# Kernel tuning notes

Hardware: AMD Instinct MI355X
Metric: run time of the kernel (lower is better)

## Reference

```python
import jax, jax.numpy as jnp
import numpy as np

N_NODES = 64
N_EDGES = N_NODES * (N_NODES - 1)  # 4032 (fully connected, no self-loops)
BATCH = 64
N_IN = 64
N_HID = 128
N_OUT = 16


def _linear_params(key, fan_in, fan_out):
    # mimic torch nn.Linear default init: U(-1/sqrt(fan_in), 1/sqrt(fan_in))
    kw, kb = jax.random.split(key)
    s = 1.0 / np.sqrt(fan_in)
    W = jax.random.uniform(kw, (fan_in, fan_out), minval=-s, maxval=s, dtype=jnp.float32)
    b = jax.random.uniform(kb, (fan_out,), minval=-s, maxval=s, dtype=jnp.float32)
    return W, b


def setup_inputs() -> dict:
    key = jax.random.key(0)
    ks = jax.random.split(key, 10)
    # one-hot relation matrices for fully-connected graph without self loops
    pairs = np.array([(i, j) for i in range(N_NODES) for j in range(N_NODES) if i != j])
    eye = np.eye(N_NODES, dtype=np.float32)
    rel_send = jnp.asarray(eye[pairs[:, 0]])  # [E, N]
    rel_rec = jnp.asarray(eye[pairs[:, 1]])   # [E, N]

    x = jax.random.normal(ks[0], (BATCH, N_NODES, N_IN), dtype=jnp.float32)

    w1a, b1a = _linear_params(ks[1], N_IN, N_HID)
    w1b, b1b = _linear_params(ks[2], N_HID, N_HID)
    w2a, b2a = _linear_params(ks[3], 2 * N_HID, N_HID)
    w2b, b2b = _linear_params(ks[4], N_HID, N_HID)
    w3a, b3a = _linear_params(ks[5], N_HID, N_HID)
    w3b, b3b = _linear_params(ks[6], N_HID, N_HID)
    w4a, b4a = _linear_params(ks[7], 3 * N_HID, N_HID)  # factor=True
    w4b, b4b = _linear_params(ks[8], N_HID, N_HID)
    wout, bout = _linear_params(ks[9], N_HID, N_OUT)

    return dict(x=x, rel_rec=rel_rec, rel_send=rel_send,
                w1a=w1a, b1a=b1a, w1b=w1b, b1b=b1b,
                w2a=w2a, b2a=b2a, w2b=w2b, b2b=b2b,
                w3a=w3a, b3a=b3a, w3b=w3b, b3b=b3b,
                w4a=w4a, b4a=b4a, w4b=w4b, b4b=b4b,
                wout=wout, bout=bout)


def _mlp(x, wa, ba, wb, bb):
    # Linear -> ReLU -> Linear
    return jax.nn.relu(x @ wa + ba) @ wb + bb


def reference(x, rel_rec, rel_send,
              w1a, b1a, w1b, b1b,
              w2a, b2a, w2b, b2b,
              w3a, b3a, w3b, b3b,
              w4a, b4a, w4b, b4b,
              wout, bout):
    def node2edge(h):
        receivers = jnp.einsum('en,bnh->beh', rel_rec, h)
        senders = jnp.einsum('en,bnh->beh', rel_send, h)
        return jnp.concatenate([senders, receivers], axis=-1)  # [B,E,2H]

    def edge2node(e):
        agg = jnp.einsum('en,beh->bnh', rel_rec, e)
        norm = rel_rec.sum(0)[None, :, None]  # [1,N,1]
        return agg / (norm + 1e-6)

    h = _mlp(x, w1a, b1a, w1b, b1b)            # [B,N,H]
    e = _mlp(node2edge(h), w2a, b2a, w2b, b2b)  # [B,E,H]
    x_skip = e
    # factor=True branch
    n = _mlp(edge2node(e), w3a, b3a, w3b, b3b)  # [B,N,H]
    e2 = node2edge(n)                           # [B,E,2H]
    e2 = jnp.concatenate([e2, x_skip], axis=2)  # [B,E,3H]
    e2 = _mlp(e2, w4a, b4a, w4b, b4b)           # [B,E,H]
    return e2 @ wout + bout                     # [B,E,n_out]
```

## Files before the change

### kernel.cpp

```cpp
#include <hip/hip_runtime.h>
#include <hip/hip_bf16.h>


#define DI __device__ __forceinline__

typedef short bf16x8 __attribute__((ext_vector_type(8)));
typedef float f32x4 __attribute__((ext_vector_type(4)));
typedef unsigned short u16;
typedef unsigned long long u64;

static constexpr int NN = 64, NE = 4032, H = 128;

DI u16 f2bf(float f) {
  union { float f; unsigned u; } v; v.f = f;
  unsigned u = v.u;
  return (u16)((u + 0x7fffu + ((u >> 16) & 1u)) >> 16);
}
DI unsigned pk2(float a, float b) {
  union { __hip_bfloat162 h; unsigned u; } c;
  c.h = __float22bfloat162_rn(float2{a, b});
  return c.u;
}
DI f32x4 mf(bf16x8 a, bf16x8 b, f32x4 c) {
  return __builtin_amdgcn_mfma_f32_16x16x32_bf16(a, b, c, 0, 0, 0);
}
DI bf16x8 ldfrag(const u16* __restrict__ p, int idx, int l) {
  return *reinterpret_cast<const bf16x8*>(p + (idx * 64 + l) * 8);
}

__global__ __launch_bounds__(64) void prepack_kernel(
    const float* __restrict__ w1a, const float* __restrict__ w1b,
    const float* __restrict__ w2a, const float* __restrict__ w2b,
    const float* __restrict__ w3a, const float* __restrict__ w3b,
    const float* __restrict__ w4a, const float* __restrict__ w4b,
    const float* __restrict__ wout,
    const float* __restrict__ b2b, const float* __restrict__ b4b,
    const float* __restrict__ bout,
    u16* __restrict__ pk, float* __restrict__ c2, float* __restrict__ c4) {
  int seg = blockIdx.y, f = blockIdx.x, l = threadIdx.x;
  int h = l >> 4, mm = l & 15;
  if (seg == 10) {
    if (f >= 4) return;
    union { u16 u[8]; uint4 q; } o;
#pragma unroll
    for (int jj = 0; jj < 8; jj++) {
      int row = f * 32 + h * 8 + jj;
      float s0 = 0.f, s1 = 0.f, s2 = 0.f, s3 = 0.f;
      for (int j = 0; j < 128; j += 4) {
        s0 += w4b[row * 128 + j]     * wout[j * 16 + mm];
        s1 += w4b[row * 128 + j + 1] * wout[(j + 1) * 16 + mm];
        s2 += w4b[row * 128 + j + 2] * wout[(j + 2) * 16 + mm];
        s3 += w4b[row * 128 + j + 3] * wout[(j + 3) * 16 + mm];
      }
      o.u[jj] = f2bf((s0 + s1) + (s2 + s3));
    }
    *reinterpret_cast<uint4*>(pk + ((304 + f) * 64 + l) * 8) = o.q;
    return;
  }
  if (seg == 11) {
    if (f < 2) {
      int o = f * 64 + l;
      float s0 = 0.f, s1 = 0.f;
      for (int k = 0; k < 128; k += 2) {
        s0 += b2b[k] * w4a[(256 + k) * 128 + o];
        s1 += b2b[k + 1] * w4a[(256 + k + 1) * 128 + o];
      }
      c2[o] = s0 + s1;
    } else if (f == 2 && l < 16) {
      float s = bout[l];
      for (int k = 0; k < 128; k++) s += b4b[k] * wout[k * 16 + l];
      c4[l] = s;
    }
    return;
  }
  const float* src; int foff, nfrag, roff, pi;
  switch (seg) {
    case 0:  src = w1a; foff = 0;   nfrag = 16; roff = 0;   pi = 0; break;
    case 1:  src = w1b; foff = 16;  nfrag = 32; roff = 0;   pi = 1; break;
    case 2:  src = w2a; foff = 48;  nfrag = 32; roff = 0;   pi = 1; break;
    case 3:  src = w2a; foff = 80;  nfrag = 32; roff = 128; pi = 1; break;
    case 4:  src = w2b; foff = 112; nfrag = 32; roff = 0;   pi = 0; break;
    case 5:  src = w3a; foff = 144; nfrag = 32; roff = 0;   pi = 1; break;
    case 6:  src = w3b; foff = 176; nfrag = 32; roff = 0;   pi = 1; break;
    case 7:  src = w4a; foff = 208; nfrag = 32; roff = 0;   pi = 1; break;
    case 8:  src = w4a; foff = 240; nfrag = 32; roff = 128; pi = 1; break;
    default: src = w4a; foff = 272; nfrag = 32; roff = 256; pi = 0; break;
  }
  if (f >= nfrag) return;
  int kt = f >> 3, ct = f & 7;
  union { u16 u[8]; uint4 q; } o;
#pragma unroll
  for (int jj = 0; jj < 8; jj++) {
    int row = pi ? (kt * 32 + (jj >> 2) * 16 + h * 4 + (jj & 3))
                 : (kt * 32 + h * 8 + jj);
    o.u[jj] = f2bf(src[(roff + row) * 128 + ct * 16 + mm]);
  }
  *reinterpret_cast<uint4*>(pk + ((foff + f) * 64 + l) * 8) = o.q;
}

__global__ __launch_bounds__(512, 2) void node_kernel(
    const float* __restrict__ x, const u16* __restrict__ pk,
    const float* __restrict__ b1a, const float* __restrict__ b1b,
    const float* __restrict__ b2a,
    float* __restrict__ sproj, float* __restrict__ rproj) {
  __shared__ bf16x8 act[2][4][64];
  int blk = blockIdx.x, b = blk >> 2, nq = blk & 3;
  int tid = threadIdx.x, l = tid & 63, w = tid >> 6;
  int m = l & 15, h = l >> 4;
  int node = nq * 16 + m;
  const f32x4 Z = {0.f, 0.f, 0.f, 0.f};
  bf16x8 wpre[14];
  wpre[0] = ldfrag(pk, w, l);
  wpre[1] = ldfrag(pk, 8 + w, l);
#pragma unroll
  for (int kt = 0; kt < 4; kt++) {
    wpre[2 + kt]  = ldfrag(pk + 16 * 512, kt * 8 + w, l);
    wpre[6 + kt]  = ldfrag(pk + 48 * 512, kt * 8 + w, l);
    wpre[10 + kt] = ldfrag(pk + 80 * 512, kt * 8 + w, l);
  }
  f32x4 acc;
  {
    const float* xb = x + (b * NN + node) * 64;
    bf16x8 xin[2];
#pragma unroll
    for (int kt = 0; kt < 2; kt++) {
      f32x4 a0 = *(const f32x4*)(xb + kt * 32 + h * 8);
      f32x4 a1 = *(const f32x4*)(xb + kt * 32 + h * 8 + 4);
      union { unsigned u[4]; bf16x8 v; } t;
      t.u[0] = pk2(a0[0], a0[1]); t.u[1] = pk2(a0[2], a0[3]);
      t.u[2] = pk2(a1[0], a1[1]); t.u[3] = pk2(a1[2], a1[3]);
      xin[kt] = t.v;
    }
    acc = mf(wpre[0], xin[0], Z);
    acc = mf(wpre[1], xin[1], acc);
    f32x4 bb = *(const f32x4*)(b1a + w * 16 + h * 4);
    union { unsigned u[2]; u64 d; } p;
    p.u[0] = pk2(fmaxf(acc[0] + bb[0], 0.f), fmaxf(acc[1] + bb[1], 0.f));
    p.u[1] = pk2(fmaxf(acc[2] + bb[2], 0.f), fmaxf(acc[3] + bb[3], 0.f));
    reinterpret_cast<u64*>(&act[0][w >> 1][l])[w & 1] = p.d;
  }
  __syncthreads();
  bf16x8 ef[4];
#pragma unroll
  for (int kt = 0; kt < 4; kt++) ef[kt] = act[0][kt][l];
#pragma unroll
  for (int kt = 0; kt < 4; kt++)
    acc = mf(wpre[2 + kt], ef[kt], kt == 0 ? Z : acc);
  {
    f32x4 bb = *(const f32x4*)(b1b + w * 16 + h * 4);
    union { unsigned u[2]; u64 d; } p;
    p.u[0] = pk2(acc[0] + bb[0], acc[1] + bb[1]);
    p.u[1] = pk2(acc[2] + bb[2], acc[3] + bb[3]);
    reinterpret_cast<u64*>(&act[1][w >> 1][l])[w & 1] = p.d;
  }
  __syncthreads();
#pragma unroll
  for (int kt = 0; kt < 4; kt++) ef[kt] = act[1][kt][l];
#pragma unroll
  for (int kt = 0; kt < 4; kt++)
    acc = mf(wpre[6 + kt], ef[kt], kt == 0 ? Z : acc);
  *reinterpret_cast<f32x4*>(sproj + (b * NN + node) * H + w * 16 + h * 4) = acc;
#pragma unroll
  for (int kt = 0; kt < 4; kt++)
    acc = mf(wpre[10 + kt], ef[kt], kt == 0 ? Z : acc);
  {
    f32x4 bb = *(const f32x4*)(b2a + w * 16 + h * 4);
    f32x4 o = acc;
    o[0] += bb[0]; o[1] += bb[1]; o[2] += bb[2]; o[3] += bb[3];
    *reinterpret_cast<f32x4*>(rproj + (b * NN + node) * H + w * 16 + h * 4) = o;
  }
}

__global__ __launch_bounds__(512, 2) void agg_kernel(
    const float* __restrict__ sproj, const float* __restrict__ rproj,
    const u16* __restrict__ pk,
    const float* __restrict__ b2b, const float* __restrict__ b3a,
    const float* __restrict__ b3b, const float* __restrict__ b4a,
    const float* __restrict__ c2,
    float* __restrict__ s4, float* __restrict__ r4) {
  __shared__ f32x4 lred[8][8][64];
  __shared__ bf16x8 act[2][4][64];
  int blk = blockIdx.x, b = blk >> 2, jq = blk & 3;
  int tid = threadIdx.x, l = tid & 63, w = tid >> 6, m = l & 15, h = l >> 4;
  int j = jq * 16 + m;
  const float* rpb = rproj + (b * NN + j) * H;
  f32x4 rpv[8], accS[8];
#pragma unroll
  for (int k = 0; k < 8; k++) {
    rpv[k] = *(const f32x4*)(rpb + (k >> 1) * 32 + h * 8 + (k & 1) * 4);
    accS[k] = f32x4{0.f, 0.f, 0.f, 0.f};
  }
  const float* spb = sproj + b * NN * H;
  for (int i = w * 8; i < w * 8 + 8; i++) {
    const float* sp = spb + i * H;
#pragma unroll
    for (int k = 0; k < 8; k++) {
      f32x4 s = *(const f32x4*)(sp + (k >> 1) * 32 + h * 8 + (k & 1) * 4);
      f32x4 t = s + rpv[k];
      t[0] = fmaxf(t[0], 0.f); t[1] = fmaxf(t[1], 0.f);
      t[2] = fmaxf(t[2], 0.f); t[3] = fmaxf(t[3], 0.f);
      accS[k] += t;
    }
  }
  if ((j >> 3) == w) {
    const float* sp = spb + j * H;
#pragma unroll
    for (int k = 0; k < 8; k++) {
      f32x4 s = *(const f32x4*)(sp + (k >> 1) * 32 + h * 8 + (k & 1) * 4);
      f32x4 t = s + rpv[k];
      accS[k][0] -= fmaxf(t[0], 0.f); accS[k][1] -= fmaxf(t[1], 0.f);
      accS[k][2] -= fmaxf(t[2], 0.f); accS[k][3] -= fmaxf(t[3], 0.f);
    }
  }
#pragma unroll
  for (int k = 0; k < 8; k++) lred[w][k][l] = accS[k];
  bf16x8 wpre[20];
#pragma unroll
  for (int kt = 0; kt < 4; kt++) {
    wpre[kt]      = ldfrag(pk + 112 * 512, kt * 8 + w, l);
    wpre[4 + kt]  = ldfrag(pk + 144 * 512, kt * 8 + w, l);
    wpre[8 + kt]  = ldfrag(pk + 176 * 512, kt * 8 + w, l);
    wpre[12 + kt] = ldfrag(pk + 208 * 512, kt * 8 + w, l);
    wpre[16 + kt] = ldfrag(pk + 240 * 512, kt * 8 + w, l);
  }
  __syncthreads();
  if (w < 4) {
    f32x4 s0 = f32x4{0.f, 0.f, 0.f, 0.f}, s1 = s0;
#pragma unroll
    for (int ww = 0; ww < 8; ww++) {
      s0 += lred[ww][2 * w][l];
      s1 += lred[ww][2 * w + 1][l];
    }
    union { unsigned u[4]; bf16x8 v; } t;
    t.u[0] = pk2(s0[0], s0[1]); t.u[1] = pk2(s0[2], s0[3]);
    t.u[2] = pk2(s1[0], s1[1]); t.u[3] = pk2(s1[2], s1[3]);
    act[0][w][l] = t.v;
  }
  __syncthreads();
  const f32x4 Z = {0.f, 0.f, 0.f, 0.f};
  f32x4 acc;
  bf16x8 ef[4];
#pragma unroll
  for (int kt = 0; kt < 4; kt++) ef[kt] = act[0][kt][l];
#pragma unroll
  for (int kt = 0; kt < 4; kt++)
    acc = mf(wpre[kt], ef[kt], kt == 0 ? Z : acc);
  {
    const float inv = 1.0f / (63.0f + 1e-6f);
    const float binv = 63.0f * inv;
    f32x4 bb = *(const f32x4*)(b2b + w * 16 + h * 4);
    union { unsigned u[2]; u64 d; } p;
    p.u[0] = pk2(acc[0] * inv + bb[0] * binv, acc[1] * inv + bb[1] * binv);
    p.u[1] = pk2(acc[2] * inv + bb[2] * binv, acc[3] * inv + bb[3] * binv);
    reinterpret_cast<u64*>(&act[1][w >> 1][l])[w & 1] = p.d;
  }
  __syncthreads();
#pragma unroll
  for (int kt = 0; kt < 4; kt++) ef[kt] = act[1][kt][l];
#pragma unroll
  for (int kt = 0; kt < 4; kt++)
    acc = mf(wpre[4 + kt], ef[kt], kt == 0 ? Z : acc);
  {
    f32x4 bb = *(const f32x4*)(b3a + w * 16 + h * 4);
    union { unsigned u[2]; u64 d; } p;
    p.u[0] = pk2(fmaxf(acc[0] + bb[0], 0.f), fmaxf(acc[1] + bb[1], 0.f));
    p.u[1] = pk2(fmaxf(acc[2] + bb[2], 0.f), fmaxf(acc[3] + bb[3], 0.f));
    reinterpret_cast<u64*>(&act[0][w >> 1][l])[w & 1] = p.d;
  }
  __syncthreads();
#pragma unroll
  for (int kt = 0; kt < 4; kt++) ef[kt] = act[0][kt][l];
#pragma unroll
  for (int kt = 0; kt < 4; kt++)
    acc = mf(wpre[8 + kt], ef[kt], kt == 0 ? Z : acc);
  {
    f32x4 bb = *(const f32x4*)(b3b + w * 16 + h * 4);
    union { unsigned u[2]; u64 d; } p;
    p.u[0] = pk2(acc[0] + bb[0], acc[1] + bb[1]);
    p.u[1] = pk2(acc[2] + bb[2], acc[3] + bb[3]);
    reinterpret_cast<u64*>(&act[1][w >> 1][l])[w & 1] = p.d;
  }
  __syncthreads();
#pragma unroll
  for (int kt = 0; kt < 4; kt++) ef[kt] = act[1][kt][l];
#pragma unroll
  for (int kt = 0; kt < 4; kt++)
    acc = mf(wpre[12 + kt], ef[kt], kt == 0 ? Z : acc);
  {
    f32x4 cc = *(const f32x4*)(c2 + w * 16 + h * 4);
    f32x4 o = acc;
    o[0] += cc[0]; o[1] += cc[1]; o[2] += cc[2]; o[3] += cc[3];
    *reinterpret_cast<f32x4*>(s4 + (b * NN + j) * H + w * 16 + h * 4) = o;
  }
#pragma unroll
  for (int kt = 0; kt < 4; kt++)
    acc = mf(wpre[16 + kt], ef[kt], kt == 0 ? Z : acc);
  {
    f32x4 bb = *(const f32x4*)(b4a + w * 16 + h * 4);
    f32x4 o = acc;
    o[0] += bb[0]; o[1] += bb[1]; o[2] += bb[2]; o[3] += bb[3];
    *reinterpret_cast<f32x4*>(r4 + (b * NN + j) * H + w * 16 + h * 4) = o;
  }
}

__global__ __launch_bounds__(256, 4) void edge_kernel(
    const float* __restrict__ sproj, const float* __restrict__ rproj,
    const float* __restrict__ s4, const float* __restrict__ r4,
    const u16* __restrict__ pk, const float* __restrict__ c4,
    float* __restrict__ out) {
  __shared__ alignas(16) u16 bufA[8192];
  __shared__ alignas(16) u16 bufB[8192];
  int blk = blockIdx.x;
  int wg = (blk & 7) * 512 + (blk >> 3);
  int b = wg >> 6, i = wg & 63;
  int tid = threadIdx.x, l = tid & 63, w = tid >> 6;
  int m16 = l & 15, h = l >> 4;
  const f32x4 Z = {0.f, 0.f, 0.f, 0.f};
  int jnv[4];
#pragma unroll
  for (int n = 0; n < 4; n++) {
    int e = n * 16 + m16;
    int v = e + (e >= i ? 1 : 0); jnv[n] = v > 63 ? 63 : v;
  }
  {
    const float* spp = sproj + (b * NN + i) * H + w * 32 + h * 8;
    f32x4 s0 = *(const f32x4*)spp, s1 = *(const f32x4*)(spp + 4);
#pragma unroll
    for (int n = 0; n < 4; n++) {
      const float* rpp = rproj + (b * NN + jnv[n]) * H + w * 32 + h * 8;
      f32x4 r0 = *(const f32x4*)rpp, r1 = *(const f32x4*)(rpp + 4);
      union { unsigned u[4]; uint4 q; } t;
      t.u[0] = pk2(fmaxf(s0[0] + r0[0], 0.f), fmaxf(s0[1] + r0[1], 0.f));
      t.u[1] = pk2(fmaxf(s0[2] + r0[2], 0.f), fmaxf(s0[3] + r0[3], 0.f));
      t.u[2] = pk2(fmaxf(s1[0] + r1[0], 0.f), fmaxf(s1[1] + r1[1], 0.f));
      t.u[3] = pk2(fmaxf(s1[2] + r1[2], 0.f), fmaxf(s1[3] + r1[3], 0.f));
      *reinterpret_cast<uint4*>(&bufA[((w * 4 + n) * 64 + l) * 8]) = t.q;
    }
  }
  bf16x8 wv[8];
#pragma unroll
  for (int idx = 0; idx < 8; idx++)
    wv[idx] = ldfrag(pk + 112 * 512, (idx >> 1) * 8 + 2 * w + (idx & 1), l);
  __syncthreads();
  f32x4 acc[2][4];
  __builtin_amdgcn_s_setprio(1);
#pragma unroll
  for (int n = 0; n < 4; n++) {
    bf16x8 bf[4];
#pragma unroll
    for (int kt = 0; kt < 4; kt++)
      bf[kt] = *reinterpret_cast<const bf16x8*>(&bufA[((kt * 4 + n) * 64 + l) * 8]);
#pragma unroll
    for (int kt = 0; kt < 4; kt++)
#pragma unroll
      for (int m = 0; m < 2; m++)
        acc[m][n] = mf(wv[kt * 2 + m], bf[kt], kt == 0 ? Z : acc[m][n]);
  }
  __builtin_amdgcn_s_setprio(0);
#pragma unroll
  for (int idx = 0; idx < 8; idx++)
    wv[idx] = ldfrag(pk + 272 * 512, (idx >> 1) * 8 + 2 * w + (idx & 1), l);
  {
    int lane2b = (h >> 1) * 16 + m16;
    int jb = (h & 1) * 4;
#pragma unroll
    for (int m = 0; m < 2; m++)
#pragma unroll
      for (int n = 0; n < 4; n++) {
        union { unsigned u[2]; u64 d; } p;
        p.u[0] = pk2(acc[m][n][0], acc[m][n][1]);
        p.u[1] = pk2(acc[m][n][2], acc[m][n][3]);
        *reinterpret_cast<u64*>(
            &bufB[((w * 4 + n) * 64 + lane2b + m * 32) * 8 + jb]) = p.d;
      }
  }
  f32x4 s4v[2], rv[4][2];
#pragma unroll
  for (int m = 0; m < 2; m++)
    s4v[m] = *(const f32x4*)(s4 + (b * NN + i) * H + w * 32 + m * 16 + h * 4);
#pragma unroll
  for (int n = 0; n < 4; n++) {
    const float* r4p = r4 + (b * NN + jnv[n]) * H + w * 32 + h * 4;
#pragma unroll
    for (int m = 0; m < 2; m++) rv[n][m] = *(const f32x4*)(r4p + m * 16);
  }
  __syncthreads();
  __builtin_amdgcn_s_setprio(1);
#pragma unroll
  for (int n = 0; n < 4; n++) {
    bf16x8 bf[4];
#pragma unroll
    for (int kt = 0; kt < 4; kt++)
      bf[kt] = *reinterpret_cast<const bf16x8*>(&bufB[((kt * 4 + n) * 64 + l) * 8]);
#pragma unroll
    for (int kt = 0; kt < 4; kt++)
#pragma unroll
      for (int m = 0; m < 2; m++)
        acc[m][n] = mf(wv[kt * 2 + m], bf[kt], kt == 0 ? Z : acc[m][n]);
  }
  __builtin_amdgcn_s_setprio(0);
  {
    int lane2b = (h >> 1) * 16 + m16;
    int jb = (h & 1) * 4;
#pragma unroll
    for (int n = 0; n < 4; n++)
#pragma unroll
      for (int m = 0; m < 2; m++) {
        f32x4 r = rv[n][m];
        union { unsigned u[2]; u64 d; } p;
        p.u[0] = pk2(fmaxf(acc[m][n][0] + s4v[m][0] + r[0], 0.f),
                     fmaxf(acc[m][n][1] + s4v[m][1] + r[1], 0.f));
        p.u[1] = pk2(fmaxf(acc[m][n][2] + s4v[m][2] + r[2], 0.f),
                     fmaxf(acc[m][n][3] + s4v[m][3] + r[3], 0.f));
        *reinterpret_cast<u64*>(
            &bufA[((w * 4 + n) * 64 + lane2b + m * 32) * 8 + jb]) = p.d;
      }
  }
  __syncthreads();
  {
    bf16x8 wfv[4], bf[4];
#pragma unroll
    for (int kt = 0; kt < 4; kt++) {
      wfv[kt] = ldfrag(pk + 304 * 512, kt, l);
      bf[kt] = *reinterpret_cast<const bf16x8*>(&bufA[((kt * 4 + w) * 64 + l) * 8]);
    }
    f32x4 a4 = Z;
#pragma unroll
    for (int kt = 0; kt < 4; kt++) a4 = mf(wfv[kt], bf[kt], a4);
    int jj = w * 16 + m16;
    if (jj < 63) {
      f32x4 c4v = *(const f32x4*)(c4 + h * 4);
      f32x4 o;
      o[0] = a4[0] + c4v[0]; o[1] = a4[1] + c4v[1];
      o[2] = a4[2] + c4v[2]; o[3] = a4[3] + c4v[3];
      *reinterpret_cast<f32x4*>(out + (b * NE + i * 63 + jj) * 16 + h * 4) = o;
    }
  }
}

extern "C" void kernel_launch(void* const* d_in, const int* in_sizes, int n_in,
                              void* d_out, int out_size, void* d_ws, size_t ws_size,
                              hipStream_t stream) {
  const float* x    = (const float*)d_in[0];
  const float* w1a  = (const float*)d_in[3];
  const float* b1a  = (const float*)d_in[4];
  const float* w1b  = (const float*)d_in[5];
  const float* b1b  = (const float*)d_in[6];
  const float* w2a  = (const float*)d_in[7];
  const float* b2a  = (const float*)d_in[8];
  const float* w2b  = (const float*)d_in[9];
  const float* b2b  = (const float*)d_in[10];
  const float* w3a  = (const float*)d_in[11];
  const float* b3a  = (const float*)d_in[12];
  const float* w3b  = (const float*)d_in[13];
  const float* b3b  = (const float*)d_in[14];
  const float* w4a  = (const float*)d_in[15];
  const float* b4a  = (const float*)d_in[16];
  const float* w4b  = (const float*)d_in[17];
  const float* b4b  = (const float*)d_in[18];
  const float* wout = (const float*)d_in[19];
  const float* bout = (const float*)d_in[20];
  float* out = (float*)d_out;

  float* sproj = (float*)d_ws;
  float* rproj = sproj + 524288;
  float* s4    = rproj + 524288;
  float* r4    = s4 + 524288;
  u16* pkw     = (u16*)(r4 + 524288);
  float* c2    = (float*)(pkw + 174080);
  float* c4    = c2 + 128;

  prepack_kernel<<<dim3(32, 12), 64, 0, stream>>>(
      w1a, w1b, w2a, w2b, w3a, w3b, w4a, w4b, wout, b2b, b4b, bout, pkw, c2, c4);
  node_kernel<<<256, 512, 0, stream>>>(x, pkw, b1a, b1b, b2a, sproj, rproj);
  agg_kernel<<<256, 512, 0, stream>>>(sproj, rproj, pkw, b2b, b3a, b3b, b4a, c2, s4, r4);
  edge_kernel<<<4096, 256, 0, stream>>>(sproj, rproj, s4, r4, pkw, c4, out);
}
```

Before: 83.31 us.

## Process four sender nodes per edge block with software-pipelined staging

Each edge_kernel block now handles four consecutive sender nodes in a loop instead of one, cutting the grid from 4096 to 1024 blocks. The next sender's first-layer input is loaded from global memory and written to a third LDS buffer while the current sender's second and third GEMMs run. The aim is to amortize block launch and weight-fragment setup and to hide global load latency. In exchange, LDS use rises to 48KB per block, which may lower occupancy, and there are fewer blocks to spread across CUs.

```diff
diff --git a/kernel.cpp b/kernel.cpp
--- a/kernel.cpp
+++ b/kernel.cpp
@@ -308,132 +308,164 @@
     const float* __restrict__ s4, const float* __restrict__ r4,
     const u16* __restrict__ pk, const float* __restrict__ c4,
     float* __restrict__ out) {
-  __shared__ alignas(16) u16 bufA[8192];
-  __shared__ alignas(16) u16 bufB[8192];
+  __shared__ alignas(16) u16 bufT[8192];
+  __shared__ alignas(16) u16 bufE[8192];
+  __shared__ alignas(16) u16 bufU[8192];
   int blk = blockIdx.x;
-  int wg = (blk & 7) * 512 + (blk >> 3);
-  int b = wg >> 6, i = wg & 63;
+  int wg = (blk & 7) * 128 + (blk >> 3);
+  int b = wg >> 4, sg = wg & 15;
   int tid = threadIdx.x, l = tid & 63, w = tid >> 6;
   int m16 = l & 15, h = l >> 4;
   const f32x4 Z = {0.f, 0.f, 0.f, 0.f};
-  int jnv[4];
-#pragma unroll
-  for (int n = 0; n < 4; n++) {
-    int e = n * 16 + m16;
-    int v = e + (e >= i ? 1 : 0); jnv[n] = v > 63 ? 63 : v;
-  }
-  {
-    const float* spp = sproj + (b * NN + i) * H + w * 32 + h * 8;
+  int i0 = sg * 4;
+  {
+    const float* spp = sproj + (b * NN + i0) * H + w * 32 + h * 8;
     f32x4 s0 = *(const f32x4*)spp, s1 = *(const f32x4*)(spp + 4);
 #pragma unroll
     for (int n = 0; n < 4; n++) {
-      const float* rpp = rproj + (b * NN + jnv[n]) * H + w * 32 + h * 8;
+      int e = n * 16 + m16;
+      int v = e + (e >= i0 ? 1 : 0); v = v > 63 ? 63 : v;
+      const float* rpp = rproj + (b * NN + v) * H + w * 32 + h * 8;
       f32x4 r0 = *(const f32x4*)rpp, r1 = *(const f32x4*)(rpp + 4);
       union { unsigned u[4]; uint4 q; } t;
       t.u[0] = pk2(fmaxf(s0[0] + r0[0], 0.f), fmaxf(s0[1] + r0[1], 0.f));
       t.u[1] = pk2(fmaxf(s0[2] + r0[2], 0.f), fmaxf(s0[3] + r0[3], 0.f));
       t.u[2] = pk2(fmaxf(s1[0] + r1[0], 0.f), fmaxf(s1[1] + r1[1], 0.f));
       t.u[3] = pk2(fmaxf(s1[2] + r1[2], 0.f), fmaxf(s1[3] + r1[3], 0.f));
-      *reinterpret_cast<uint4*>(&bufA[((w * 4 + n) * 64 + l) * 8]) = t.q;
-    }
-  }
-  bf16x8 wv[8];
-#pragma unroll
-  for (int idx = 0; idx < 8; idx++)
-    wv[idx] = ldfrag(pk + 112 * 512, (idx >> 1) * 8 + 2 * w + (idx & 1), l);
-  __syncthreads();
-  f32x4 acc[2][4];
-  __builtin_amdgcn_s_setprio(1);
-#pragma unroll
-  for (int n = 0; n < 4; n++) {
-    bf16x8 bf[4];
-#pragma unroll
-    for (int kt = 0; kt < 4; kt++)
-      bf[kt] = *reinterpret_cast<const bf16x8*>(&bufA[((kt * 4 + n) * 64 + l) * 8]);
-#pragma unroll
-    for (int kt = 0; kt < 4; kt++)
+      *reinterpret_cast<uint4*>(&bufT[((w * 4 + n) * 64 + l) * 8]) = t.q;
+    }
+  }
+  __syncthreads();
+#pragma unroll 1
+  for (int s = 0; s < 4; s++) {
+    int i = i0 + s;
+    int jnv[4];
+#pragma unroll
+    for (int n = 0; n < 4; n++) {
+      int e = n * 16 + m16;
+      int v = e + (e >= i ? 1 : 0); jnv[n] = v > 63 ? 63 : v;
+    }
+    f32x4 acc[2][4];
+    bf16x8 wv[8];
+#pragma unroll
+    for (int idx = 0; idx < 8; idx++)
+      wv[idx] = ldfrag(pk + 112 * 512, (idx >> 1) * 8 + 2 * w + (idx & 1), l);
+    __builtin_amdgcn_s_setprio(1);
+#pragma unroll
+    for (int n = 0; n < 4; n++) {
+      bf16x8 bf[4];
+#pragma unroll
+      for (int kt = 0; kt < 4; kt++)
+        bf[kt] = *reinterpret_cast<const bf16x8*>(&bufT[((kt * 4 + n) * 64 + l) * 8]);
+#pragma unroll
+      for (int kt = 0; kt < 4; kt++)
+#pragma unroll
+        for (int m = 0; m < 2; m++)
+          acc[m][n] = mf(wv[kt * 2 + m], bf[kt], kt == 0 ? Z : acc[m][n]);
+    }
+    __builtin_amdgcn_s_setprio(0);
+#pragma unroll
+    for (int idx = 0; idx < 8; idx++)
+      wv[idx] = ldfrag(pk + 272 * 512, (idx >> 1) * 8 + 2 * w + (idx & 1), l);
+    {
+      int lane2b = (h >> 1) * 16 + m16;
+      int jb = (h & 1) * 4;
 #pragma unroll
       for (int m = 0; m < 2; m++)
-        acc[m][n] = mf(wv[kt * 2 + m], bf[kt], kt == 0 ? Z : acc[m][n]);
-  }
-  __builtin_amdgcn_s_setprio(0);
-#pragma unroll
-  for (int idx = 0; idx < 8; idx++)
-    wv[idx] = ldfrag(pk + 272 * 512, (idx >> 1) * 8 + 2 * w + (idx & 1), l);
-  {
-    int lane2b = (h >> 1) * 16 + m16;
-    int jb = (h & 1) * 4;
+#pragma unroll
+        for (int n = 0; n < 4; n++) {
+          union { unsigned u[2]; u64 d; } p;
+          p.u[0] = pk2(acc[m][n][0], acc[m][n][1]);
+          p.u[1] = pk2(acc[m][n][2], acc[m][n][3]);
+          *reinterpret_cast<u64*>(
+              &bufE[((w * 4 + n) * 64 + lane2b + m * 32) * 8 + jb]) = p.d;
+        }
+    }
+    f32x4 ts0, ts1, tr[4][2];
+    if (s < 3) {
+      int i2 = i + 1;
+      const float* spp = sproj + (b * NN + i2) * H + w * 32 + h * 8;
+      ts0 = *(const f32x4*)spp; ts1 = *(const f32x4*)(spp + 4);
+#pragma unroll
+      for (int n = 0; n < 4; n++) {
+        int e = n * 16 + m16;
+        int v = e + (e >= i2 ? 1 : 0); v = v > 63 ? 63 : v;
+        const float* rpp = rproj + (b * NN + v) * H + w * 32 + h * 8;
+        tr[n][0] = *(const f32x4*)rpp; tr[n][1] = *(const f32x4*)(rpp + 4);
+      }
+    }
+    __syncthreads();
+    if (s < 3) {
+#pragma unroll
+      for (int n = 0; n < 4; n++) {
+        union { unsigned u[4]; uint4 q; } t;
+        t.u[0] = pk2(fmaxf(ts0[0] + tr[n][0][0], 0.f), fmaxf(ts0[1] + tr[n][0][1], 0.f));
+        t.u[1] = pk2(fmaxf(ts0[2] + tr[n][0][2], 0.f), fmaxf(ts0[3] + tr[n][0][3], 0.f));
+        t.u[2] = pk2(fmaxf(ts1[0] + tr[n][1][0], 0.f), fmaxf(ts1[1] + tr[n][1][1], 0.f));
+        t.u[3] = pk2(fmaxf(ts1[2] + tr[n][1][2], 0.f), fmaxf(ts1[3] + tr[n][1][3], 0.f));
+        *reinterpret_cast<uint4*>(&bufT[((w * 4 + n) * 64 + l) * 8]) = t.q;
+      }
+    }
+    f32x4 s4v[2], rv[4][2];
 #pragma unroll
     for (int m = 0; m < 2; m++)
-#pragma unroll
-      for (int n = 0; n < 4; n++) {
-        union { unsigned u[2]; u64 d; } p;
-        p.u[0] = pk2(acc[m][n][0], acc[m][n][1]);
-        p.u[1] = pk2(acc[m][n][2], acc[m][n][3]);
-        *reinterpret_cast<u64*>(
-            &bufB[((w * 4 + n) * 64 + lane2b + m * 32) * 8 + jb]) = p.d;
+      s4v[m] = *(const f32x4*)(s4 + (b * NN + i) * H + w * 32 + m * 16 + h * 4);
+#pragma unroll
+    for (int n = 0; n < 4; n++) {
+      const float* r4p = r4 + (b * NN + jnv[n]) * H + w * 32 + h * 4;
+#pragma unroll
+      for (int m = 0; m < 2; m++) rv[n][m] = *(const f32x4*)(r4p + m * 16);
+    }
+    __builtin_amdgcn_s_setprio(1);
+#pragma unroll
+    for (int n = 0; n < 4; n++) {
+      bf16x8 bf[4];
+#pragma unroll
+      for (int kt = 0; kt < 4; kt++)
+        bf[kt] = *reinterpret_cast<const bf16x8*>(&bufE[((kt * 4 + n) * 64 + l) * 8]);
+#pragma unroll
+      for (int kt = 0; kt < 4; kt++)
+#pragma unroll
+        for (int m = 0; m < 2; m++)
+          acc[m][n] = mf(wv[kt * 2 + m], bf[kt], kt == 0 ? Z : acc[m][n]);
+    }
+    __builtin_amdgcn_s_setprio(0);
+    {
+      int lane2b = (h >> 1) * 16 + m16;
+      int jb = (h & 1) * 4;
+#pragma unroll
+      for (int n = 0; n < 4; n++)
+#pragma unroll
+        for (int m = 0; m < 2; m++) {
+          f32x4 r = rv[n][m];
+          union { unsigned u[2]; u64 d; } p;
+          p.u[0] = pk2(fmaxf(acc[m][n][0] + s4v[m][0] + r[0], 0.f),
+                       fmaxf(acc[m][n][1] + s4v[m][1] + r[1], 0.f));
+          p.u[1] = pk2(fmaxf(acc[m][n][2] + s4v[m][2] + r[2], 0.f),
+                       fmaxf(acc[m][n][3] + s4v[m][3] + r[3], 0.f));
+          *reinterpret_cast<u64*>(
+              &bufU[((w * 4 + n) * 64 + lane2b + m * 32) * 8 + jb]) = p.d;
+        }
+    }
+    __syncthreads();
+    {
+      bf16x8 wfv[4], bf[4];
+#pragma unroll
+      for (int kt = 0; kt < 4; kt++) {
+        wfv[kt] = ldfrag(pk + 304 * 512, kt, l);
+        bf[kt] = *reinterpret_cast<const bf16x8*>(&bufU[((kt * 4 + w) * 64 + l) * 8]);
       }
-  }
-  f32x4 s4v[2], rv[4][2];
-#pragma unroll
-  for (int m = 0; m < 2; m++)
-    s4v[m] = *(const f32x4*)(s4 + (b * NN + i) * H + w * 32 + m * 16 + h * 4);
-#pragma unroll
-  for (int n = 0; n < 4; n++) {
-    const float* r4p = r4 + (b * NN + jnv[n]) * H + w * 32 + h * 4;
-#pragma unroll
-    for (int m = 0; m < 2; m++) rv[n][m] = *(const f32x4*)(r4p + m * 16);
-  }
-  __syncthreads();
-  __builtin_amdgcn_s_setprio(1);
-#pragma unroll
-  for (int n = 0; n < 4; n++) {
-    bf16x8 bf[4];
-#pragma unroll
-    for (int kt = 0; kt < 4; kt++)
-      bf[kt] = *reinterpret_cast<const bf16x8*>(&bufB[((kt * 4 + n) * 64 + l) * 8]);
-#pragma unroll
-    for (int kt = 0; kt < 4; kt++)
-#pragma unroll
-      for (int m = 0; m < 2; m++)
-        acc[m][n] = mf(wv[kt * 2 + m], bf[kt], kt == 0 ? Z : acc[m][n]);
-  }
-  __builtin_amdgcn_s_setprio(0);
-  {
-    int lane2b = (h >> 1) * 16 + m16;
-    int jb = (h & 1) * 4;
-#pragma unroll
-    for (int n = 0; n < 4; n++)
-#pragma unroll
-      for (int m = 0; m < 2; m++) {
-        f32x4 r = rv[n][m];
-        union { unsigned u[2]; u64 d; } p;
-        p.u[0] = pk2(fmaxf(acc[m][n][0] + s4v[m][0] + r[0], 0.f),
-                     fmaxf(acc[m][n][1] + s4v[m][1] + r[1], 0.f));
-        p.u[1] = pk2(fmaxf(acc[m][n][2] + s4v[m][2] + r[2], 0.f),
-                     fmaxf(acc[m][n][3] + s4v[m][3] + r[3], 0.f));
-        *reinterpret_cast<u64*>(
-            &bufA[((w * 4 + n) * 64 + lane2b + m * 32) * 8 + jb]) = p.d;
+      f32x4 a4 = Z;
+#pragma unroll
+      for (int kt = 0; kt < 4; kt++) a4 = mf(wfv[kt], bf[kt], a4);
+      int jj = w * 16 + m16;
+      if (jj < 63) {
+        f32x4 c4v = *(const f32x4*)(c4 + h * 4);
+        f32x4 o;
+        o[0] = a4[0] + c4v[0]; o[1] = a4[1] + c4v[1];
+        o[2] = a4[2] + c4v[2]; o[3] = a4[3] + c4v[3];
+        *reinterpret_cast<f32x4*>(out + (b * NE + i * 63 + jj) * 16 + h * 4) = o;
       }
-  }
-  __syncthreads();
-  {
-    bf16x8 wfv[4], bf[4];
-#pragma unroll
-    for (int kt = 0; kt < 4; kt++) {
-      wfv[kt] = ldfrag(pk + 304 * 512, kt, l);
-      bf[kt] = *reinterpret_cast<const bf16x8*>(&bufA[((kt * 4 + w) * 64 + l) * 8]);
-    }
-    f32x4 a4 = Z;
-#pragma unroll
-    for (int kt = 0; kt < 4; kt++) a4 = mf(wfv[kt], bf[kt], a4);
-    int jj = w * 16 + m16;
-    if (jj < 63) {
-      f32x4 c4v = *(const f32x4*)(c4 + h * 4);
-      f32x4 o;
-      o[0] = a4[0] + c4v[0]; o[1] = a4[1] + c4v[1];
-      o[2] = a4[2] + c4v[2]; o[3] = a4[3] + c4v[3];
-      *reinterpret_cast<f32x4*>(out + (b * NE + i * 63 + jj) * 16 + h * 4) = o;
     }
   }
 }
@@ -474,5 +506,5 @@
       w1a, w1b, w2a, w2b, w3a, w3b, w4a, w4b, wout, b2b, b4b, bout, pkw, c2, c4);
   node_kernel<<<256, 512, 0, stream>>>(x, pkw, b1a, b1b, b2a, sproj, rproj);
   agg_kernel<<<256, 512, 0, stream>>>(sproj, rproj, pkw, b2b, b3a, b3b, b4a, c2, s4, r4);
-  edge_kernel<<<4096, 256, 0, stream>>>(sproj, rproj, s4, r4, pkw, c4, out);
-}
+  edge_kernel<<<1024, 256, 0, stream>>>(sproj, rproj, s4, r4, pkw, c4, out);
+}
```

Result: no change. 84.20 us (+1.1%).
